# Performance work log

Hardware: AMD Instinct MI355X
Metric: run time of the kernel (lower is better)

Reference implementation:

```python
import jax, jax.numpy as jnp
import numpy as np

VOCAB = 10000
D = 512          # output_dim (input_size == hidden_size for SRU highway)
N_LAYERS = 4
B, S = 32, 1024


def setup_inputs() -> dict:
    key = jax.random.key(0)
    k0, k1, k2, k3 = jax.random.split(key, 4)
    ids = jax.random.randint(k0, (B, S), 0, VOCAB)
    mask = jnp.ones((B, S), dtype=bool)  # True = valid token, False = pad
    emb = jax.random.normal(k1, (VOCAB, D), jnp.float32) * 0.02
    # per-layer SRU weights: W -> [u0 | u_f | u_r], v -> (v_f, v_r) cell-coupling, b -> (b_f, b_r)
    W = jax.random.normal(k2, (N_LAYERS, D, 3 * D), jnp.float32) * (1.0 / np.sqrt(D))
    v = jax.random.normal(k3, (N_LAYERS, 2, D), jnp.float32) * 0.1
    b = jnp.zeros((N_LAYERS, 2 * D), jnp.float32)
    return {"ids": ids, "mask": mask, "emb": emb, "W": W, "v": v, "b": b}


def _sru_layer(x, W_l, v_l, b_l, pad):
    # x: [S, B, D] time-major input; pad: [S, B] bool (True at padded positions)
    # SRU (Lei et al.) with use_tanh and highway connection:
    #   f_t = sigmoid(u_f + v_f * c_{t-1} + b_f)
    #   r_t = sigmoid(u_r + v_r * c_{t-1} + b_r)
    #   c_t = f_t * c_{t-1} + (1 - f_t) * u0_t   (held at c_{t-1} where padded)
    #   h_t = r_t * tanh(c_t) + (1 - r_t) * x_t  (zeroed where padded)
    U = jnp.einsum('sbd,de->sbe', x, W_l)           # [S, B, 3D], the only GEMM
    u0, uf, ur = jnp.split(U, 3, axis=-1)
    vf, vr = v_l[0], v_l[1]
    bf, br = jnp.split(b_l, 2)
    c0 = jnp.zeros(x.shape[1:], x.dtype)             # [B, D]
    def step(c, inp):
        u0t, uft, urt, xt, pt = inp
        f = jax.nn.sigmoid(uft + vf * c + bf)
        r = jax.nn.sigmoid(urt + vr * c + br)
        c_new = f * c + (1.0 - f) * u0t
        c_new = jnp.where(pt[:, None], c, c_new)
        h = r * jnp.tanh(c_new) + (1.0 - r) * xt
        h = jnp.where(pt[:, None], 0.0, h)
        return c_new, h
    _, hs = jax.lax.scan(step, c0, (u0, uf, ur, x, pad))
    return hs  # [S, B, D]


def reference(ids, mask, emb, W, v, b):
    x = emb[ids]                       # [B, S, D] char-embedded tokens
    x = jnp.transpose(x, (1, 0, 2))    # time-major [S, B, D] (matches permute(1,0,2))
    pad = (~mask).T                    # [S, B], matches inverted_mask.T -> mask_pad
    for l in range(W.shape[0]):        # small fixed layer count
        x = _sru_layer(x, W[l], v[l], b[l], pad)
    return jnp.transpose(x, (1, 0, 2))  # back to [B, S, D]
```

## Files before the change

### kernel.cpp

```cpp
#include <hip/hip_runtime.h>
#include <cstdint>
#include <cstddef>

#define S_LEN 1024
#define B_SZ  32
#define D_DIM 512
#define N3D   1536
#define M_ROWS (S_LEN * B_SZ)
#define M_HALF (M_ROWS / 2)
#define N_LAYERS 4

typedef _Float16 f16;
typedef _Float16 half8 __attribute__((ext_vector_type(8)));
typedef float f32x16 __attribute__((ext_vector_type(16)));
typedef float f32x8 __attribute__((ext_vector_type(8)));

#define EXP2F(x) __builtin_amdgcn_exp2f(x)

typedef const __attribute__((address_space(1))) unsigned int* gp1_t;
typedef __attribute__((address_space(3))) unsigned int* lp3_t;
#define GLOAD16(g, l) __builtin_amdgcn_global_load_lds((gp1_t)(g), (lp3_t)(l), 16, 0, 0)

__device__ inline f32x16 mfma16(half8 a, half8 b, f32x16 c) {
  return __builtin_amdgcn_mfma_f32_32x32x16_f16(a, b, c, 0, 0, 0);
}

__global__ void embed_kernel(const int* __restrict__ ids,
                             const float* __restrict__ emb,
                             f16* __restrict__ Xh, f16* __restrict__ Xl) {
  int i = blockIdx.x * 256 + threadIdx.x;
  int row = i >> 6;
  int q   = i & 63;
  int s = row >> 5, b = row & 31;
  int id = ids[b * S_LEN + s];
  const float4* src = (const float4*)(emb + (size_t)id * D_DIM) + q * 2;
  float4 v0 = src[0], v1 = src[1];
  float xs[8] = {v0.x, v0.y, v0.z, v0.w, v1.x, v1.y, v1.z, v1.w};
  half8 h, lo;
  #pragma unroll
  for (int j = 0; j < 8; j++) {
    f16 hv = (f16)xs[j];
    h[j] = hv;
    lo[j] = (f16)((xs[j] - (float)hv) * 2048.0f);
  }
  *(half8*)(Xh + (size_t)row * D_DIM + q * 8) = h;
  *(half8*)(Xl + (size_t)row * D_DIM + q * 8) = lo;
}

__global__ void wsplit_kernel(const float* __restrict__ W,
                              f16* __restrict__ Bfh, f16* __restrict__ Bfl) {
  __shared__ float t[32][33];
  int l = blockIdx.z;
  int nb = blockIdx.x * 32, kb = blockIdx.y * 32;
  const float* Wl = W + (size_t)l * D_DIM * N3D;
  int tx = threadIdx.x & 31, ty = threadIdx.x >> 5;
  for (int r = ty; r < 32; r += 8)
    t[r][tx] = Wl[(size_t)(kb + r) * N3D + nb + tx];
  __syncthreads();
  if (ty < 4) {
    int kg = ty;
    half8 hv, lv;
    #pragma unroll
    for (int e = 0; e < 8; e++) {
      float x = t[kg * 8 + e][tx];
      f16 h = (f16)x;
      hv[e] = h;
      lv[e] = (f16)((x - (float)h) * 2048.0f);
    }
    size_t idx = ((size_t)l * 48 + (nb >> 5)) * 32 + (kb >> 4) + (kg >> 1);
    size_t off = idx * 512 + (size_t)(tx + 32 * (kg & 1)) * 8;
    *(half8*)(Bfh + off) = hv;
    *(half8*)(Bfl + off) = lv;
  }
}

#define SBAR()  do { __builtin_amdgcn_s_barrier(); __builtin_amdgcn_sched_barrier(0); } while (0)
#define WAITV(N) do { asm volatile("s_waitcnt vmcnt(" #N ")" ::: "memory"); \
                      __builtin_amdgcn_sched_barrier(0); } while (0)

__global__ __launch_bounds__(256, 2)
void gemm_kernel(const f16* __restrict__ Ah, const f16* __restrict__ Al,
                 const f16* __restrict__ Bfh, const f16* __restrict__ Bfl,
                 float* __restrict__ C, int m_base) {
  __shared__ char lds[49152];
  const int lane = threadIdx.x & 63, wid = threadIdx.x >> 6;
  const int wm = wid >> 1, wn = wid & 1;

  const int orig = blockIdx.x;
  const int wg = (orig & 7) * 192 + (orig >> 3);
  const int m0 = (wg / 12) * 128;
  const int n0 = (wg % 12) * 128;

  int rowA[2], boA[2];
  #pragma unroll
  for (int s = 0; s < 2; ++s) {
    int p = (wid * 2 + s) * 1024 + lane * 16;
    int e = p ^ ((p >> 2) & 0x70) ^ ((p >> 4) & 0x10);
    rowA[s] = e >> 6; boA[s] = e & 63;
  }
  const char* gAh = (const char*)Ah + (size_t)(m_base + m0) * 1024;
  const char* gAl = (const char*)Al + (size_t)(m_base + m0) * 1024;
  char* lw = (char*)lds;

  const int arow = lane & 31, kg = lane >> 5;
  const int swz = (arow & 7) << 4;
  const int aoff0 = (((wm * 64 + arow) * 64) + kg * 16) ^ swz;
  const int aoff1 = (((wm * 64 + 32 + arow) * 64) + kg * 16) ^ swz;

  const char* gBh = (const char*)Bfh + ((size_t)((n0 >> 5) + wn * 2) << 15) + lane * 16;
  const char* gBl = (const char*)Bfl + ((size_t)((n0 >> 5) + wn * 2) << 15) + lane * 16;

  f32x16 ch00 = {0}, ch01 = {0}, ch10 = {0}, ch11 = {0};
  f32x16 cx00 = {0}, cx01 = {0}, cx10 = {0}, cx11 = {0};

#define STAGE(KT, BUF)                                                          \
  do {                                                                          \
    size_t ko_ = (size_t)(KT) * 64;                                             \
    GLOAD16(gAh + (size_t)rowA[0] * 1024 + ko_ + boA[0], lw + (BUF) + (wid * 2 + 0) * 1024); \
    GLOAD16(gAh + (size_t)rowA[1] * 1024 + ko_ + boA[1], lw + (BUF) + (wid * 2 + 1) * 1024); \
    GLOAD16(gAl + (size_t)rowA[0] * 1024 + ko_ + boA[0], lw + (BUF) + 8192 + (wid * 2 + 0) * 1024); \
    GLOAD16(gAl + (size_t)rowA[1] * 1024 + ko_ + boA[1], lw + (BUF) + 8192 + (wid * 2 + 1) * 1024); \
  } while (0)

  STAGE(0, 0);
  __builtin_amdgcn_sched_barrier(0);
  half8 cb0h = *(const half8*)(gBh + 0);
  half8 cb1h = *(const half8*)(gBh + 32768);
  half8 cb0l = *(const half8*)(gBl + 0);
  half8 cb1l = *(const half8*)(gBl + 32768);
  __builtin_amdgcn_sched_barrier(0);
  STAGE(1, 16384);

  #pragma unroll
  for (int kt = 0; kt < 16; ++kt) {
    const int cb = (kt % 3) * 16384;
    WAITV(8);
    SBAR();
    half8 nb0h = cb0h, nb1h = cb1h, nb0l = cb0l, nb1l = cb1l;
    if (kt < 15) {
      const size_t kn_ = (size_t)((kt + 1) * 2) * 1024;
      nb0h = *(const half8*)(gBh + kn_);
      nb1h = *(const half8*)(gBh + 32768 + kn_);
      nb0l = *(const half8*)(gBl + kn_);
      nb1l = *(const half8*)(gBl + 32768 + kn_);
    }
    const size_t k1_ = (size_t)(kt * 2 + 1) * 1024;
    half8 e0h = *(const half8*)(gBh + k1_);
    half8 e1h = *(const half8*)(gBh + 32768 + k1_);
    half8 e0l = *(const half8*)(gBl + k1_);
    half8 e1l = *(const half8*)(gBl + 32768 + k1_);
    __builtin_amdgcn_sched_barrier(0);
    if (kt < 14) STAGE(kt + 2, ((kt + 2) % 3) * 16384);
    __builtin_amdgcn_sched_barrier(0);

    {
      half8 a_h0 = *(const half8*)(lw + cb + aoff0);
      half8 a_h1 = *(const half8*)(lw + cb + aoff1);
      half8 a_l0 = *(const half8*)(lw + cb + 8192 + aoff0);
      half8 a_l1 = *(const half8*)(lw + cb + 8192 + aoff1);
      __builtin_amdgcn_s_setprio(1);
      ch00 = mfma16(a_h0, cb0h, ch00);
      ch01 = mfma16(a_h0, cb1h, ch01);
      ch10 = mfma16(a_h1, cb0h, ch10);
      ch11 = mfma16(a_h1, cb1h, ch11);
      cx00 = mfma16(a_h0, cb0l, cx00);
      cx01 = mfma16(a_h0, cb1l, cx01);
      cx10 = mfma16(a_h1, cb0l, cx10);
      cx11 = mfma16(a_h1, cb1l, cx11);
      cx00 = mfma16(a_l0, cb0h, cx00);
      cx01 = mfma16(a_l0, cb1h, cx01);
      cx10 = mfma16(a_l1, cb0h, cx10);
      cx11 = mfma16(a_l1, cb1h, cx11);
      __builtin_amdgcn_s_setprio(0);
    }
    {
      half8 a_h0 = *(const half8*)(lw + cb + (aoff0 ^ 32));
      half8 a_h1 = *(const half8*)(lw + cb + (aoff1 ^ 32));
      half8 a_l0 = *(const half8*)(lw + cb + 8192 + (aoff0 ^ 32));
      half8 a_l1 = *(const half8*)(lw + cb + 8192 + (aoff1 ^ 32));
      __builtin_amdgcn_s_setprio(1);
      ch00 = mfma16(a_h0, e0h, ch00);
      ch01 = mfma16(a_h0, e1h, ch01);
      ch10 = mfma16(a_h1, e0h, ch10);
      ch11 = mfma16(a_h1, e1h, ch11);
      cx00 = mfma16(a_h0, e0l, cx00);
      cx01 = mfma16(a_h0, e1l, cx01);
      cx10 = mfma16(a_h1, e0l, cx10);
      cx11 = mfma16(a_h1, e1l, cx11);
      cx00 = mfma16(a_l0, e0h, cx00);
      cx01 = mfma16(a_l0, e1h, cx01);
      cx10 = mfma16(a_l1, e0h, cx10);
      cx11 = mfma16(a_l1, e1h, cx11);
      __builtin_amdgcn_s_setprio(0);
    }
    cb0h = nb0h; cb1h = nb1h; cb0l = nb0l; cb1l = nb1l;
  }
#undef STAGE

  const int ccol = lane & 31, crow4 = 4 * (lane >> 5);
  const float inv = 1.0f / 2048.0f;
#define EPI(CH, CX, I, J)                                                       \
  do {                                                                          \
    float* cp = C + (size_t)(m0 + wm * 64 + (I) * 32) * N3D + n0 + wn * 64 + (J) * 32 + ccol; \
    _Pragma("unroll")                                                           \
    for (int g = 0; g < 4; ++g)                                                 \
      _Pragma("unroll")                                                         \
      for (int q = 0; q < 4; ++q) {                                             \
        int row = crow4 + 8 * g + q;                                            \
        cp[(size_t)row * N3D] = CH[g * 4 + q] + CX[g * 4 + q] * inv;            \
      }                                                                         \
  } while (0)
  EPI(ch00, cx00, 0, 0); EPI(ch01, cx01, 0, 1);
  EPI(ch10, cx10, 1, 0); EPI(ch11, cx11, 1, 1);
#undef EPI
}

#define LOADF(dst, ptr) asm volatile("global_load_dword %0, %1, off" : "=v"(dst) : "v"(ptr))
#define CWAIT(N)                                                      \
  do { asm volatile("s_waitcnt vmcnt(" #N ")" ::: "memory");          \
       __builtin_amdgcn_sched_barrier(0); } while (0)

__global__ __launch_bounds__(64, 1)
void cchain_kernel(const float* __restrict__ U, float* __restrict__ Carr,
                   const float* __restrict__ vparam, const float* __restrict__ bparam,
                   float* __restrict__ cstate, int layer, int tbeg, int tcnt) {
  int b = blockIdx.x >> 3;
  int d = (blockIdx.x & 7) * 64 + threadIdx.x;

  const float kL = -1.44269504088896f;
  float vfk = vparam[layer * 1024 + d] * kL;
  float bf  = bparam[layer * 1024 + d];
  float c = (tbeg == 0) ? 0.f : cstate[b * D_DIM + d];

  const size_t stepU = (size_t)B_SZ * N3D;
  const size_t stepC = (size_t)B_SZ * D_DIM;
  const float* pU = U + (size_t)b * N3D + d;
  float* pC = Carr + ((size_t)tbeg * B_SZ + b) * D_DIM + d;

  float u0a[8], ufa[8], u0b[8], ufb[8];

#define CISSUE(SFX, T0)                                               \
  do {                                                                \
    int ts_ = ((T0) < tcnt) ? (T0) : 0;                               \
    const float* q_ = pU + (size_t)ts_ * stepU;                       \
    _Pragma("unroll")                                                 \
    for (int j = 0; j < 8; j++) {                                     \
      LOADF(u0##SFX[j], q_ + (size_t)j * stepU);                      \
      LOADF(uf##SFX[j], q_ + (size_t)j * stepU + 512);                \
    }                                                                 \
  } while (0)

#define CCOMP(SFX, T0)                                                \
  do {                                                                \
    float base_[8];                                                   \
    _Pragma("unroll")                                                 \
    for (int j = 0; j < 8; j++) base_[j] = (uf##SFX[j] + bf) * kL;    \
    _Pragma("unroll")                                                 \
    for (int j = 0; j < 8; j++) {                                     \
      float e = EXP2F(__builtin_fmaf(vfk, c, base_[j]));              \
      float num = __builtin_fmaf(u0##SFX[j], e, c);                   \
      c = __fdividef(num, e + 1.0f);                                  \
      pC[(size_t)((T0) + j) * stepC] = c;                             \
    }                                                                 \
  } while (0)

  CISSUE(a, 0);
  CISSUE(b, 8);
  CWAIT(16);
  CCOMP(a, 0); CISSUE(a, 16);
  for (int t0 = 8; t0 + 8 < tcnt; t0 += 16) {
    CWAIT(24);
    CCOMP(b, t0); CISSUE(b, t0 + 16);
    CWAIT(24);
    CCOMP(a, t0 + 8); CISSUE(a, t0 + 24);
  }
  CWAIT(24);
  CCOMP(b, tcnt - 8);

  cstate[b * D_DIM + d] = c;
#undef CISSUE
#undef CCOMP
}

template <int LAST>
__global__ __launch_bounds__(256)
void hout_kernel(const float* __restrict__ U, const float* __restrict__ Carr,
                 f16* Xh, f16* Xl, float* __restrict__ OUT,
                 const float* __restrict__ vparam, const float* __restrict__ bparam,
                 int layer, int tbeg) {
  int g = blockIdx.x * 256 + threadIdx.x;
  int d8 = (g & 63) * 8;
  int b  = (g >> 6) & 31;
  int t  = g >> 11;
  int tg = tbeg + t;

  size_t urow = (size_t)(t * B_SZ + b) * N3D + 1024 + d8;
  size_t crow = (size_t)(tg * B_SZ + b) * D_DIM + d8;

  f32x8 ur = *(const f32x8*)(U + urow);
  f32x8 ct = *(const f32x8*)(Carr + crow);
  f32x8 cp = {};
  if (tg != 0) cp = *(const f32x8*)(Carr + crow - (size_t)B_SZ * D_DIM);
  half8 xh = *(const half8*)(Xh + crow);
  half8 xl = *(const half8*)(Xl + crow);
  f32x8 vr = *(const f32x8*)(vparam + layer * 1024 + 512 + d8);
  f32x8 br = *(const f32x8*)(bparam + layer * 1024 + 512 + d8);

  f32x8 hv;
  #pragma unroll
  for (int j = 0; j < 8; j++) {
    float s = __builtin_fmaf(vr[j], cp[j], ur[j]) + br[j];
    float er = EXP2F(s * -1.44269504f);
    float r = __fdividef(1.f, 1.f + er);
    float e2 = EXP2F(ct[j] * 2.88539008f);
    float th = 1.f - __fdividef(2.f, e2 + 1.f);
    float x = (float)xh[j] + (float)xl[j] * (1.f / 2048.f);
    hv[j] = x + r * (th - x);
  }

  if (LAST) {
    size_t orow = ((size_t)b * S_LEN + tg) * D_DIM + d8;
    *(f32x8*)(OUT + orow) = hv;
  } else {
    half8 oh, ol;
    #pragma unroll
    for (int j = 0; j < 8; j++) {
      f16 hh = (f16)hv[j];
      oh[j] = hh;
      ol[j] = (f16)((hv[j] - (float)hh) * 2048.0f);
    }
    *(half8*)(Xh + crow) = oh;
    *(half8*)(Xl + crow) = ol;
  }
}

extern "C" void kernel_launch(void* const* d_in, const int* in_sizes, int n_in,
                              void* d_out, int out_size, void* d_ws, size_t ws_size,
                              hipStream_t stream) {
  (void)in_sizes; (void)n_in; (void)out_size; (void)ws_size;
  const int*   ids = (const int*)d_in[0];
  const float* emb = (const float*)d_in[2];
  const float* W   = (const float*)d_in[3];
  const float* v   = (const float*)d_in[4];
  const float* b   = (const float*)d_in[5];
  float* out = (float*)d_out;

  char* ws = (char*)d_ws;
  float* U    = (float*)ws;
  f16*   Xh   = (f16*)(ws + (size_t)100663296);
  f16*   Xl   = (f16*)(ws + (size_t)134217728);
  f16*   Bfh  = (f16*)(ws + (size_t)167772160);
  f16*   Bfl  = (f16*)(ws + (size_t)174063616);
  float* cst  = (float*)(ws + (size_t)180355072);
  float* Carr = (float*)(ws + (size_t)180420608);

  wsplit_kernel<<<dim3(N3D / 32, D_DIM / 32, N_LAYERS), 256, 0, stream>>>(W, Bfh, Bfl);
  embed_kernel<<<dim3(M_ROWS * 64 / 256), 256, 0, stream>>>(ids, emb, Xh, Xl);

  const size_t wlsz = (size_t)N3D * D_DIM;
  for (int l = 0; l < N_LAYERS; ++l) {
    for (int h = 0; h < 2; ++h) {
      gemm_kernel<<<dim3(1536), 256, 0, stream>>>(
          Xh, Xl, Bfh + (size_t)l * wlsz, Bfl + (size_t)l * wlsz, U, h * M_HALF);
      cchain_kernel<<<dim3(256), 64, 0, stream>>>(U, Carr, v, b, cst,
                                                  l, h * (S_LEN / 2), S_LEN / 2);
      if (l < N_LAYERS - 1)
        hout_kernel<0><<<dim3(4096), 256, 0, stream>>>(U, Carr, Xh, Xl, nullptr,
                                                       v, b, l, h * (S_LEN / 2));
      else
        hout_kernel<1><<<dim3(4096), 256, 0, stream>>>(U, Carr, Xh, Xl, out,
                                                       v, b, l, h * (S_LEN / 2));
    }
  }
}
```

Before: 1.138 ms.

## Fuse the highway output computation into the serial recurrence scan kernel

Replaces the separate cchain and hout kernels with one scan kernel. It computes the r gate, tanh and the highway output per timestep and writes h (as split fp16 or as fp32 output) directly. This removes the fp32 C-array round trip through global memory and one launch per layer-half. In exchange, the latency-bound per-thread serial scan (only 256 blocks of 64 threads) now issues extra loads (u_r and the x hi/lo halves) and extra math per step. Its prefetch depth drops from 8 to 4 timesteps per buffer, so it may hide memory latency less well.

```diff
diff --git a/kernel.cpp b/kernel.cpp
--- a/kernel.cpp
+++ b/kernel.cpp
@@ -13,7 +13,6 @@
 typedef _Float16 f16;
 typedef _Float16 half8 __attribute__((ext_vector_type(8)));
 typedef float f32x16 __attribute__((ext_vector_type(16)));
-typedef float f32x8 __attribute__((ext_vector_type(8)));
 
 #define EXP2F(x) __builtin_amdgcn_exp2f(x)
 
@@ -216,122 +215,105 @@
 }
 
 #define LOADF(dst, ptr) asm volatile("global_load_dword %0, %1, off" : "=v"(dst) : "v"(ptr))
-#define CWAIT(N)                                                      \
-  do { asm volatile("s_waitcnt vmcnt(" #N ")" ::: "memory");          \
-       __builtin_amdgcn_sched_barrier(0); } while (0)
-
+#define LOADH(dst, ptr) asm volatile("global_load_ushort %0, %1, off" : "=v"(dst) : "v"(ptr))
+
+template <int LAST>
 __global__ __launch_bounds__(64, 1)
-void cchain_kernel(const float* __restrict__ U, float* __restrict__ Carr,
-                   const float* __restrict__ vparam, const float* __restrict__ bparam,
-                   float* __restrict__ cstate, int layer, int tbeg, int tcnt) {
+void scan_kernel(const float* __restrict__ U,
+                 f16* __restrict__ Xh, f16* __restrict__ Xl,
+                 float* __restrict__ OUT,
+                 const float* __restrict__ vparam, const float* __restrict__ bparam,
+                 float* __restrict__ cstate, int layer, int tbeg, int tcnt) {
   int b = blockIdx.x >> 3;
   int d = (blockIdx.x & 7) * 64 + threadIdx.x;
 
   const float kL = -1.44269504088896f;
   float vfk = vparam[layer * 1024 + d] * kL;
+  float vrk = vparam[layer * 1024 + 512 + d] * kL;
   float bf  = bparam[layer * 1024 + d];
+  float br  = bparam[layer * 1024 + 512 + d];
   float c = (tbeg == 0) ? 0.f : cstate[b * D_DIM + d];
 
   const size_t stepU = (size_t)B_SZ * N3D;
-  const size_t stepC = (size_t)B_SZ * D_DIM;
+  const size_t stepX = (size_t)B_SZ * D_DIM;
   const float* pU = U + (size_t)b * N3D + d;
-  float* pC = Carr + ((size_t)tbeg * B_SZ + b) * D_DIM + d;
-
-  float u0a[8], ufa[8], u0b[8], ufb[8];
+  f16* pXh = Xh + ((size_t)tbeg * B_SZ + b) * D_DIM + d;
+  f16* pXl = Xl + ((size_t)tbeg * B_SZ + b) * D_DIM + d;
+  float* pO = OUT + ((size_t)b * S_LEN + tbeg) * D_DIM + d;
+  const float invs = 1.0f / 2048.0f;
+
+  float u0a[4], ufa[4], ura[4], u0b[4], ufb[4], urb[4];
+  unsigned xha[4], xla[4], xhb[4], xlb[4];
 
 #define CISSUE(SFX, T0)                                               \
   do {                                                                \
     int ts_ = ((T0) < tcnt) ? (T0) : 0;                               \
     const float* q_ = pU + (size_t)ts_ * stepU;                       \
+    const f16* qh_ = pXh + (size_t)ts_ * stepX;                       \
+    const f16* ql_ = pXl + (size_t)ts_ * stepX;                       \
     _Pragma("unroll")                                                 \
-    for (int j = 0; j < 8; j++) {                                     \
+    for (int j = 0; j < 4; j++) {                                     \
       LOADF(u0##SFX[j], q_ + (size_t)j * stepU);                      \
       LOADF(uf##SFX[j], q_ + (size_t)j * stepU + 512);                \
+      LOADF(ur##SFX[j], q_ + (size_t)j * stepU + 1024);               \
+      LOADH(xh##SFX[j], qh_ + (size_t)j * stepX);                     \
+      LOADH(xl##SFX[j], ql_ + (size_t)j * stepX);                     \
     }                                                                 \
+  } while (0)
+
+#define CWAITP() do { asm volatile("s_waitcnt vmcnt(20)" ::: "memory"); \
+                      __builtin_amdgcn_sched_barrier(0); } while (0)
+#define CWAITS()                                                      \
+  do {                                                                \
+    if (LAST) asm volatile("s_waitcnt vmcnt(24)" ::: "memory");       \
+    else      asm volatile("s_waitcnt vmcnt(28)" ::: "memory");       \
+    __builtin_amdgcn_sched_barrier(0);                                \
   } while (0)
 
 #define CCOMP(SFX, T0)                                                \
   do {                                                                \
-    float base_[8];                                                   \
     _Pragma("unroll")                                                 \
-    for (int j = 0; j < 8; j++) base_[j] = (uf##SFX[j] + bf) * kL;    \
-    _Pragma("unroll")                                                 \
-    for (int j = 0; j < 8; j++) {                                     \
-      float e = EXP2F(__builtin_fmaf(vfk, c, base_[j]));              \
-      float num = __builtin_fmaf(u0##SFX[j], e, c);                   \
-      c = __fdividef(num, e + 1.0f);                                  \
-      pC[(size_t)((T0) + j) * stepC] = c;                             \
+    for (int j = 0; j < 4; j++) {                                     \
+      float x = (float)__builtin_bit_cast(_Float16, (unsigned short)xh##SFX[j]) \
+              + (float)__builtin_bit_cast(_Float16, (unsigned short)xl##SFX[j]) * invs; \
+      float basef = (uf##SFX[j] + bf) * kL;                           \
+      float baser = (ur##SFX[j] + br) * kL;                           \
+      float cold = c;                                                 \
+      float ef = EXP2F(__builtin_fmaf(vfk, cold, basef));             \
+      c = __fdividef(__builtin_fmaf(u0##SFX[j], ef, cold), ef + 1.f); \
+      float er = EXP2F(__builtin_fmaf(vrk, cold, baser));             \
+      float r = __fdividef(1.f, 1.f + er);                            \
+      float e2 = EXP2F(c * 2.88539008f);                              \
+      float th = 1.f - __fdividef(2.f, e2 + 1.f);                     \
+      float h = x + r * (th - x);                                     \
+      if (LAST) {                                                     \
+        pO[(size_t)((T0) + j) * D_DIM] = h;                           \
+      } else {                                                        \
+        f16 hh = (f16)h;                                              \
+        pXh[(size_t)((T0) + j) * stepX] = hh;                         \
+        pXl[(size_t)((T0) + j) * stepX] = (f16)((h - (float)hh) * 2048.0f); \
+      }                                                               \
     }                                                                 \
   } while (0)
 
   CISSUE(a, 0);
-  CISSUE(b, 8);
-  CWAIT(16);
-  CCOMP(a, 0); CISSUE(a, 16);
-  for (int t0 = 8; t0 + 8 < tcnt; t0 += 16) {
-    CWAIT(24);
-    CCOMP(b, t0); CISSUE(b, t0 + 16);
-    CWAIT(24);
-    CCOMP(a, t0 + 8); CISSUE(a, t0 + 24);
-  }
-  CWAIT(24);
-  CCOMP(b, tcnt - 8);
+  CISSUE(b, 4);
+  CWAITP();
+  CCOMP(a, 0); CISSUE(a, 8);
+  for (int t0 = 4; t0 + 4 < tcnt; t0 += 8) {
+    CWAITS();
+    CCOMP(b, t0); CISSUE(b, t0 + 8);
+    CWAITS();
+    CCOMP(a, t0 + 4); CISSUE(a, t0 + 12);
+  }
+  CWAITS();
+  CCOMP(b, tcnt - 4);
 
   cstate[b * D_DIM + d] = c;
 #undef CISSUE
+#undef CWAITP
+#undef CWAITS
 #undef CCOMP
-}
-
-template <int LAST>
-__global__ __launch_bounds__(256)
-void hout_kernel(const float* __restrict__ U, const float* __restrict__ Carr,
-                 f16* Xh, f16* Xl, float* __restrict__ OUT,
-                 const float* __restrict__ vparam, const float* __restrict__ bparam,
-                 int layer, int tbeg) {
-  int g = blockIdx.x * 256 + threadIdx.x;
-  int d8 = (g & 63) * 8;
-  int b  = (g >> 6) & 31;
-  int t  = g >> 11;
-  int tg = tbeg + t;
-
-  size_t urow = (size_t)(t * B_SZ + b) * N3D + 1024 + d8;
-  size_t crow = (size_t)(tg * B_SZ + b) * D_DIM + d8;
-
-  f32x8 ur = *(const f32x8*)(U + urow);
-  f32x8 ct = *(const f32x8*)(Carr + crow);
-  f32x8 cp = {};
-  if (tg != 0) cp = *(const f32x8*)(Carr + crow - (size_t)B_SZ * D_DIM);
-  half8 xh = *(const half8*)(Xh + crow);
-  half8 xl = *(const half8*)(Xl + crow);
-  f32x8 vr = *(const f32x8*)(vparam + layer * 1024 + 512 + d8);
-  f32x8 br = *(const f32x8*)(bparam + layer * 1024 + 512 + d8);
-
-  f32x8 hv;
-  #pragma unroll
-  for (int j = 0; j < 8; j++) {
-    float s = __builtin_fmaf(vr[j], cp[j], ur[j]) + br[j];
-    float er = EXP2F(s * -1.44269504f);
-    float r = __fdividef(1.f, 1.f + er);
-    float e2 = EXP2F(ct[j] * 2.88539008f);
-    float th = 1.f - __fdividef(2.f, e2 + 1.f);
-    float x = (float)xh[j] + (float)xl[j] * (1.f / 2048.f);
-    hv[j] = x + r * (th - x);
-  }
-
-  if (LAST) {
-    size_t orow = ((size_t)b * S_LEN + tg) * D_DIM + d8;
-    *(f32x8*)(OUT + orow) = hv;
-  } else {
-    half8 oh, ol;
-    #pragma unroll
-    for (int j = 0; j < 8; j++) {
-      f16 hh = (f16)hv[j];
-      oh[j] = hh;
-      ol[j] = (f16)((hv[j] - (float)hh) * 2048.0f);
-    }
-    *(half8*)(Xh + crow) = oh;
-    *(half8*)(Xl + crow) = ol;
-  }
 }
 
 extern "C" void kernel_launch(void* const* d_in, const int* in_sizes, int n_in,
@@ -352,7 +334,6 @@
   f16*   Bfh  = (f16*)(ws + (size_t)167772160);
   f16*   Bfl  = (f16*)(ws + (size_t)174063616);
   float* cst  = (float*)(ws + (size_t)180355072);
-  float* Carr = (float*)(ws + (size_t)180420608);
 
   wsplit_kernel<<<dim3(N3D / 32, D_DIM / 32, N_LAYERS), 256, 0, stream>>>(W, Bfh, Bfl);
   embed_kernel<<<dim3(M_ROWS * 64 / 256), 256, 0, stream>>>(ids, emb, Xh, Xl);
@@ -362,14 +343,12 @@
     for (int h = 0; h < 2; ++h) {
       gemm_kernel<<<dim3(1536), 256, 0, stream>>>(
           Xh, Xl, Bfh + (size_t)l * wlsz, Bfl + (size_t)l * wlsz, U, h * M_HALF);
-      cchain_kernel<<<dim3(256), 64, 0, stream>>>(U, Carr, v, b, cst,
-                                                  l, h * (S_LEN / 2), S_LEN / 2);
       if (l < N_LAYERS - 1)
-        hout_kernel<0><<<dim3(4096), 256, 0, stream>>>(U, Carr, Xh, Xl, nullptr,
-                                                       v, b, l, h * (S_LEN / 2));
+        scan_kernel<0><<<dim3(256), 64, 0, stream>>>(U, Xh, Xl, out, v, b, cst,
+                                                     l, h * (S_LEN / 2), S_LEN / 2);
       else
-        hout_kernel<1><<<dim3(4096), 256, 0, stream>>>(U, Carr, Xh, Xl, out,
-                                                       v, b, l, h * (S_LEN / 2));
-    }
-  }
-}
+        scan_kernel<1><<<dim3(256), 64, 0, stream>>>(U, Xh, Xl, out, v, b, cst,
+                                                     l, h * (S_LEN / 2), S_LEN / 2);
+    }
+  }
+}
```

New measurement: 1.348 ms. 18.5% more time.
